# Performance work log

Measured on AMD Instinct MI355X. Metric: run time of the kernel, lower is better.

## Reference

```python
import jax, jax.numpy as jnp
import numpy as np

LORA_SCALING = 2.0


def setup_inputs() -> dict:
    key = jax.random.key(0)
    ks = jax.random.split(key, 12)
    B, S, H, F, E, R = 1, 2048, 2048, 8192, 8, 16
    s = 0.02  # small init so lora deltas stay numerically sane
    return {
        "hidden_states": jax.random.normal(ks[0], (B, S, H), jnp.float32),
        "gate_w": jax.random.normal(ks[1], (E, H), jnp.float32) * s,
        "Wg": jax.random.normal(ks[2], (F, H), jnp.float32) * s,
        "Wu": jax.random.normal(ks[3], (F, H), jnp.float32) * s,
        "Wd": jax.random.normal(ks[4], (H, F), jnp.float32) * s,
        "Ag": jax.random.normal(ks[5], (E, R, H), jnp.float32) * s,
        "Bg": jax.random.normal(ks[6], (E, F, R), jnp.float32) * s,
        "Au": jax.random.normal(ks[7], (E, R, H), jnp.float32) * s,
        "Bu": jax.random.normal(ks[8], (E, F, R), jnp.float32) * s,
        "Ad": jax.random.normal(ks[9], (E, R, F), jnp.float32) * s,
        "Bd": jax.random.normal(ks[10], (E, H, R), jnp.float32) * s,
        "top_k": 2,
    }


def reference(hidden_states, gate_w, Wg, Wu, Wd, Ag, Bg, Au, Bu, Ad, Bd, top_k):
    B, S, H = hidden_states.shape
    E = gate_w.shape[0]
    h = hidden_states.reshape(-1, H)  # [T, H]
    # router: softmax -> top-k -> renormalize
    logits = h @ gate_w.T                       # [T, E]
    rw = jax.nn.softmax(logits, axis=-1)
    rw_top, sel = jax.lax.top_k(rw, top_k)      # [T, K]
    rw_top = rw_top / jnp.sum(rw_top, axis=-1, keepdims=True)
    # per-token per-expert combine weight (0 if expert not selected)
    w_te = jnp.zeros((h.shape[0], E), h.dtype).at[
        jnp.arange(h.shape[0])[:, None], sel].add(rw_top)  # [T, E]
    # shared base projections computed once for all experts
    common_gate = h @ Wg.T   # [T, F]
    common_up = h @ Wu.T     # [T, F]
    out = jnp.zeros_like(h)
    for e in range(E):  # small fixed expert count; lora deltas are rank-16
        g = common_gate + LORA_SCALING * ((h @ Ag[e].T) @ Bg[e].T)
        u = common_up + LORA_SCALING * ((h @ Au[e].T) @ Bu[e].T)
        act = jax.nn.silu(g) * u                               # [T, F]
        d = act @ Wd.T + LORA_SCALING * ((act @ Ad[e].T) @ Bd[e].T)  # [T, H]
        out = out + w_te[:, e:e + 1] * d
    return out.reshape(B, S, H)
```

## Files before the change

### kernel.cpp

```cpp
#include <hip/hip_runtime.h>
#include <hip/hip_bf16.h>

typedef __attribute__((ext_vector_type(8))) short v8s;
typedef __attribute__((ext_vector_type(4))) float v4f;
typedef unsigned short u16;

static constexpr int TT = 2048;
static constexpr int HD = 2048;
static constexpr int FD = 8192;
static constexpr int NE = 8;
static constexpr int NR = 16;
static constexpr int NXE = 2*FD;
static constexpr int CU_OFF = FD;
static constexpr int KXD = FD + 512;

__device__ __forceinline__ u16 f2b(float f) {
  union { float f; unsigned u; } v; v.f = f;
  unsigned r = v.u + 0x7FFFu + ((v.u >> 16) & 1u);
  return (u16)(r >> 16);
}
__device__ __forceinline__ float b2f(u16 h) {
  union { unsigned u; float f; } v; v.u = ((unsigned)h) << 16;
  return v.f;
}
__device__ __forceinline__ v8s pack8(v4f a, v4f b) {
  v8s r;
  r[0]=(short)f2b(a.x); r[1]=(short)f2b(a.y); r[2]=(short)f2b(a.z); r[3]=(short)f2b(a.w);
  r[4]=(short)f2b(b.x); r[5]=(short)f2b(b.y); r[6]=(short)f2b(b.z); r[7]=(short)f2b(b.w);
  return r;
}
__device__ __forceinline__ void gload_lds16(const void* g, void* l) {
  __builtin_amdgcn_global_load_lds(
      (const __attribute__((address_space(1))) unsigned int*)g,
      (__attribute__((address_space(3))) unsigned int*)l, 16, 0, 0);
}
__device__ __forceinline__ void barrier_pin() {
  __builtin_amdgcn_s_barrier();
  __builtin_amdgcn_sched_barrier(0);
}
__device__ __forceinline__ void vm_wait4() { asm volatile("s_waitcnt vmcnt(4)" ::: "memory"); }
__device__ __forceinline__ void vm_wait0() { asm volatile("s_waitcnt vmcnt(0)" ::: "memory"); }

template<int Q>
__device__ __forceinline__ void mmq(v4f (&acc)[8][4], const v8s (&af)[2][2], const v8s (&bf)[4][2]) {
  __builtin_amdgcn_s_setprio(1);
  #pragma unroll
  for (int m2 = 0; m2 < 2; ++m2)
    #pragma unroll
    for (int nf = 0; nf < 4; ++nf) {
      acc[Q*2+m2][nf] = __builtin_amdgcn_mfma_f32_16x16x32_bf16(af[m2][0], bf[nf][0], acc[Q*2+m2][nf], 0, 0, 0);
      acc[Q*2+m2][nf] = __builtin_amdgcn_mfma_f32_16x16x32_bf16(af[m2][1], bf[nf][1], acc[Q*2+m2][nf], 0, 0, 0);
    }
  __builtin_amdgcn_s_setprio(0);
}

static constexpr int PREP_BLOCKS = 14592;
__global__ __launch_bounds__(256)
void prep_kernel(const float* __restrict__ h, const float* __restrict__ Wg,
                 const float* __restrict__ Wu, const float* __restrict__ Wd,
                 const float* __restrict__ Ag, const float* __restrict__ Au,
                 const float* __restrict__ Bg, const float* __restrict__ Bu,
                 const float* __restrict__ Ad, const float* __restrict__ Bd,
                 u16* __restrict__ hb, u16* __restrict__ Bgux, u16* __restrict__ Agu,
                 u16* __restrict__ Wdx, u16* __restrict__ Bgb, u16* __restrict__ Bub,
                 u16* __restrict__ Adb, float* __restrict__ hAx) {
  const int b = blockIdx.x, tid = threadIdx.x;
  auto cast16 = [&](const float* s, u16* d, long blk) {
    long i = blk*4096 + (long)tid*16;
    v4f a0 = *(const v4f*)(s+i),    a1 = *(const v4f*)(s+i+4);
    v4f a2 = *(const v4f*)(s+i+8),  a3 = *(const v4f*)(s+i+12);
    *(v8s*)(d+i)   = pack8(a0, a1);
    *(v8s*)(d+i+8) = pack8(a2, a3);
  };
  if (b < 1024) { cast16(h, hb, b); }
  else if (b < 5120)  { cast16(Wg, Bgux, b-1024); }
  else if (b < 9216)  { cast16(Wu, Bgux + (size_t)FD*HD, b-5120); }
  else if (b < 13312) {
    long idx = (long)(b-9216)*4096 + (long)tid*16;
    long r = idx >> 13; int c = (int)(idx & 8191);
    const float* s = Wd + r*FD + c;
    u16* d = Wdx + r*KXD + c;
    v4f a0 = *(const v4f*)s,     a1 = *(const v4f*)(s+4);
    v4f a2 = *(const v4f*)(s+8), a3 = *(const v4f*)(s+12);
    *(v8s*)d     = pack8(a0, a1);
    *(v8s*)(d+8) = pack8(a2, a3);
  }
  else if (b < 13376) { cast16(Ag, Agu, b-13312); }
  else if (b < 13440) { cast16(Au, Agu + (size_t)128*HD, b-13376); }
  else if (b < 13696) { cast16(Bg, Bgb, b-13440); }
  else if (b < 13952) { cast16(Bu, Bub, b-13696); }
  else if (b < 14208) { cast16(Ad, Adb, b-13952); }
  else if (b < 14464) {
    long idx = (long)(b-14208)*4096 + (long)tid*16;
    int hrow = (int)(idx >> 9); int c = (int)(idx & 511);
    u16* d = Wdx + (size_t)hrow*KXD + FD + c;
    if (c < 128) {
      const float* s = Bd + ((size_t)(c>>4)*HD + hrow)*16;
      v4f a0 = *(const v4f*)s,     a1 = *(const v4f*)(s+4);
      v4f a2 = *(const v4f*)(s+8), a3 = *(const v4f*)(s+12);
      *(v8s*)d     = pack8(a0, a1);
      *(v8s*)(d+8) = pack8(a2, a3);
    } else {
      v8s z = {0,0,0,0,0,0,0,0};
      *(v8s*)d = z; *(v8s*)(d+8) = z;
    }
  } else {
    long i = (long)(b-14464)*4096 + (long)tid*16;
    v4f z = {0.f,0.f,0.f,0.f};
    *(v4f*)(hAx+i) = z; *(v4f*)(hAx+i+4) = z;
    *(v4f*)(hAx+i+8) = z; *(v4f*)(hAx+i+12) = z;
  }
}

__global__ __launch_bounds__(64)
void router_kernel(const float* __restrict__ h, const float* __restrict__ gw,
                   int* __restrict__ sel, int* __restrict__ count,
                   int* __restrict__ listTok, float* __restrict__ listW) {
  int t = blockIdx.x, lane = threadIdx.x;
  const float* hp = h + (size_t)t * HD;
  float acc[8] = {0,0,0,0,0,0,0,0};
  for (int i = lane; i < HD; i += 64) {
    float hv = hp[i];
    #pragma unroll
    for (int e = 0; e < 8; ++e) acc[e] += hv * gw[e*HD + i];
  }
  #pragma unroll
  for (int off = 32; off > 0; off >>= 1) {
    #pragma unroll
    for (int e = 0; e < 8; ++e) acc[e] += __shfl_xor(acc[e], off, 64);
  }
  if (lane == 0) {
    int e0 = -1, e1 = -1; float b0 = -1e30f, b1 = -1e30f;
    #pragma unroll
    for (int e = 0; e < 8; ++e) {
      float v = acc[e];
      if (v > b0) { b1 = b0; e1 = e0; b0 = v; e0 = e; }
      else if (v > b1) { b1 = v; e1 = e; }
    }
    float p1 = __expf(b1 - b0);
    float w0 = 1.f / (1.f + p1);
    float w1 = p1 * w0;
    sel[2*t] = e0; sel[2*t+1] = e1;
    int pos0 = atomicAdd(&count[e0], 1);
    listTok[e0*TT + pos0] = t;           listW[e0*TT + pos0] = w0;
    int pos1 = atomicAdd(&count[e1], 1);
    listTok[e1*TT + pos1] = t | (1<<20); listW[e1*TT + pos1] = w1;
  }
}

__global__ __launch_bounds__(256)
void gemm128a(const u16* __restrict__ A, const u16* __restrict__ B, float* __restrict__ Cout,
              int K, int ldc) {
  __shared__ u16 As[128*64];
  __shared__ u16 Bs[128*64];
  const int tid  = threadIdx.x;
  const int lane = tid & 63, wid = tid >> 6;
  const int gx = gridDim.x;
  const int lin = blockIdx.y * gx + blockIdx.x;
  const int chunk = (gx * gridDim.y) >> 3;
  const int wg = (lin & 7) * chunk + (lin >> 3);
  const int m0 = (wg % gx) * 128, n0 = (wg / gx) * 128;
  const int kc = K / gridDim.z;
  const int kbeg = blockIdx.z * kc;
  const int wr = wid >> 1, wc = wid & 1;
  const int lrow = lane >> 3, lcol = (lane & 7) * 8;
  v4f acc[4][4];
  #pragma unroll
  for (int mi = 0; mi < 4; ++mi)
    #pragma unroll
    for (int ni = 0; ni < 4; ++ni) acc[mi][ni] = (v4f){0.f,0.f,0.f,0.f};

  for (int k0 = kbeg; k0 < kbeg + kc; k0 += 64) {
    #pragma unroll
    for (int it = 0; it < 4; ++it) {
      int seg = wid*4 + it;
      int row = seg*8 + lrow;
      gload_lds16(A + (size_t)(m0+row)*K + k0 + lcol, As + seg*512);
      gload_lds16(B + (size_t)(n0+row)*K + k0 + lcol, Bs + seg*512);
    }
    __syncthreads();
    #pragma unroll
    for (int kk = 0; kk < 64; kk += 32) {
      v8s af[4], bfr[4];
      #pragma unroll
      for (int mi = 0; mi < 4; ++mi)
        af[mi] = *(const v8s*)(As + (wr*64 + mi*16 + (lane&15))*64 + kk + (lane>>4)*8);
      #pragma unroll
      for (int ni = 0; ni < 4; ++ni)
        bfr[ni] = *(const v8s*)(Bs + (wc*64 + ni*16 + (lane&15))*64 + kk + (lane>>4)*8);
      #pragma unroll
      for (int mi = 0; mi < 4; ++mi)
        #pragma unroll
        for (int ni = 0; ni < 4; ++ni)
          acc[mi][ni] = __builtin_amdgcn_mfma_f32_16x16x32_bf16(af[mi], bfr[ni], acc[mi][ni], 0, 0, 0);
    }
    __syncthreads();
  }

  #pragma unroll
  for (int mi = 0; mi < 4; ++mi)
    #pragma unroll
    for (int j = 0; j < 4; ++j) {
      int row = m0 + wr*64 + mi*16 + (lane>>4)*4 + j;
      size_t base = (size_t)row*ldc + n0 + wc*64 + (lane&15);
      #pragma unroll
      for (int ni = 0; ni < 4; ++ni)
        atomicAdd(&Cout[base + ni*16], acc[mi][ni][j]);
    }
}

template<int MODE>
__global__ __launch_bounds__(512, 2)
void gemm256(const u16* __restrict__ A, const u16* __restrict__ B, void* __restrict__ Cout,
             int ldk, int kchunk, int ldc) {
  __shared__ u16 lds[2][2][2][8192];
  const int tid = threadIdx.x, lane = tid & 63, wid = tid >> 6;
  const int gx = gridDim.x;
  const int nwg = gx * gridDim.y;
  const int lin = blockIdx.y * gx + blockIdx.x;
  const int chunk = nwg >> 3;
  const int wg = (lin & 7) * chunk + (lin >> 3);
  const int m0 = (wg % gx) * 256, n0 = (wg / gx) * 256;
  const long kbeg = (long)blockIdx.z * kchunk;
  const int NK = kchunk >> 6, NI = NK >> 1;
  const int wr = wid >> 2, wc = wid & 3;

  const int s_r = (wid << 4) + (lane >> 3);
  const int s_c = lane & 7;

  auto STAGE = [&](int slot, int ab, int half, const u16* M, int rc0, int kt) {
    const u16* g0 = M + (size_t)(rc0 + half*128 + s_r) * ldk + kbeg + kt*64 + ((s_c ^ (s_r & 7)) << 3);
    gload_lds16(g0, &lds[slot][ab][half][wid << 10]);
    const int r1 = s_r + 8;
    const u16* g1 = M + (size_t)(rc0 + half*128 + r1) * ldk + kbeg + kt*64 + ((s_c ^ (r1 & 7)) << 3);
    gload_lds16(g1, &lds[slot][ab][half][(wid << 10) + 512]);
  };
  auto LDA = [&](int slot, int mf, int c16b) -> v8s {
    int rr = (mf << 4) + (lane & 15);
    return *(const v8s*)&lds[slot][0][wr][rr*64 + (((c16b + (lane >> 4)) ^ (rr & 7)) << 3)];
  };
  auto LDB = [&](int slot, int nf, int c16b) -> v8s {
    int row = (wc << 6) + (nf << 4) + (lane & 15);
    int rr = row & 127;
    return *(const v8s*)&lds[slot][1][row >> 7][rr*64 + (((c16b + (lane >> 4)) ^ (rr & 7)) << 3)];
  };

  v4f acc[8][4];
  #pragma unroll
  for (int mf = 0; mf < 8; ++mf)
    #pragma unroll
    for (int nf = 0; nf < 4; ++nf) acc[mf][nf] = (v4f){0.f,0.f,0.f,0.f};

  STAGE(0,1,0,B,n0,0); STAGE(0,1,1,B,n0,0);
  STAGE(0,0,0,A,m0,0); STAGE(0,0,1,A,m0,0);
  STAGE(1,1,0,B,n0,1); STAGE(1,1,1,B,n0,1);
  vm_wait4();
  barrier_pin();

  for (int i = 0; i < NI; ++i) {
    const int kt0 = 2*i, kt1 = kt0 + 1;
    const int kt2c = (kt0 + 2 < NK) ? kt0 + 2 : kt0;
    const bool s45 = (kt0 + 2 < NK), s67 = (kt1 + 2 < NK);
    v8s bf[4][2], af[2][2];
    #pragma unroll
    for (int nf = 0; nf < 4; ++nf) { bf[nf][0] = LDB(0,nf,0); bf[nf][1] = LDB(0,nf,4); }
    af[0][0]=LDA(0,0,0); af[0][1]=LDA(0,0,4); af[1][0]=LDA(0,1,0); af[1][1]=LDA(0,1,4);
    STAGE(1,0,0,A,m0,kt1);
    barrier_pin(); mmq<0>(acc,af,bf); barrier_pin();
    af[0][0]=LDA(0,2,0); af[0][1]=LDA(0,2,4); af[1][0]=LDA(0,3,0); af[1][1]=LDA(0,3,4);
    STAGE(1,0,1,A,m0,kt1);
    barrier_pin(); mmq<1>(acc,af,bf); barrier_pin();
    af[0][0]=LDA(0,4,0); af[0][1]=LDA(0,4,4); af[1][0]=LDA(0,5,0); af[1][1]=LDA(0,5,4);
    STAGE(0,1,0,B,n0,kt2c);
    barrier_pin(); mmq<2>(acc,af,bf); barrier_pin();
    af[0][0]=LDA(0,6,0); af[0][1]=LDA(0,6,4); af[1][0]=LDA(0,7,0); af[1][1]=LDA(0,7,4);
    STAGE(0,1,1,B,n0,kt2c);
    vm_wait4();
    barrier_pin(); mmq<3>(acc,af,bf); barrier_pin();
    #pragma unroll
    for (int nf = 0; nf < 4; ++nf) { bf[nf][0] = LDB(1,nf,0); bf[nf][1] = LDB(1,nf,4); }
    af[0][0]=LDA(1,0,0); af[0][1]=LDA(1,0,4); af[1][0]=LDA(1,1,0); af[1][1]=LDA(1,1,4);
    if (s45) STAGE(0,0,0,A,m0,kt0+2);
    barrier_pin(); mmq<0>(acc,af,bf); barrier_pin();
    af[0][0]=LDA(1,2,0); af[0][1]=LDA(1,2,4); af[1][0]=LDA(1,3,0); af[1][1]=LDA(1,3,4);
    if (s45) STAGE(0,0,1,A,m0,kt0+2);
    barrier_pin(); mmq<1>(acc,af,bf); barrier_pin();
    af[0][0]=LDA(1,4,0); af[0][1]=LDA(1,4,4); af[1][0]=LDA(1,5,0); af[1][1]=LDA(1,5,4);
    if (s67) STAGE(1,1,0,B,n0,kt1+2);
    barrier_pin(); mmq<2>(acc,af,bf); barrier_pin();
    af[0][0]=LDA(1,6,0); af[0][1]=LDA(1,6,4); af[1][0]=LDA(1,7,0); af[1][1]=LDA(1,7,4);
    if (s67) STAGE(1,1,1,B,n0,kt1+2);
    vm_wait4();
    barrier_pin(); mmq<3>(acc,af,bf); barrier_pin();
  }
  vm_wait0();

  if (MODE == 0) {
    u16* C = (u16*)Cout;
    #pragma unroll
    for (int mf = 0; mf < 8; ++mf)
      #pragma unroll
      for (int j = 0; j < 4; ++j) {
        int row = m0 + wr*128 + mf*16 + (lane>>4)*4 + j;
        size_t base = (size_t)row*ldc + n0 + wc*64 + (lane&15);
        #pragma unroll
        for (int nf = 0; nf < 4; ++nf)
          C[base + nf*16] = f2b(acc[mf][nf][j]);
      }
  } else {
    float* C = (float*)Cout + (size_t)blockIdx.z * TT * HD;
    #pragma unroll
    for (int mf = 0; mf < 8; ++mf)
      #pragma unroll
      for (int j = 0; j < 4; ++j) {
        int row = m0 + wr*128 + mf*16 + (lane>>4)*4 + j;
        size_t base = (size_t)row*ldc + n0 + wc*64 + (lane&15);
        #pragma unroll
        for (int nf = 0; nf < 4; ++nf)
          C[base + nf*16] = acc[mf][nf][j];
      }
  }
}

__global__ __launch_bounds__(256)
void reduce4_kernel(const float* __restrict__ P, float* __restrict__ out) {
  long i = ((long)blockIdx.x * 256 + threadIdx.x) * 4;
  const size_t S = (size_t)TT * HD;
  v4f s = *(const v4f*)(P + i);
  s = s + *(const v4f*)(P + S + i);
  s = s + *(const v4f*)(P + 2*S + i);
  s = s + *(const v4f*)(P + 3*S + i);
  *(v4f*)(out + i) = s;
}

static constexpr int HA_LD = 40;
static constexpr int AW_LD = 72;
static constexpr int CT_LD = 72;

__global__ __launch_bounds__(256)
void expert_kernel(const u16* __restrict__ CGU,
                   const float* __restrict__ hAx,
                   const u16* __restrict__ Bgb, const u16* __restrict__ Bub,
                   const u16* __restrict__ Adb,
                   const int* __restrict__ count, const int* __restrict__ listTok,
                   const float* __restrict__ listW,
                   u16* __restrict__ actw0, u16* __restrict__ actw1,
                   float* __restrict__ cC) {
  const int e = blockIdx.y, g = blockIdx.x, fb = blockIdx.z;
  const int n = count[e];
  if (g*16 >= n) return;
  const int tid = threadIdx.x, lane = tid & 63, w = tid >> 6;
  __shared__ u16 hAg[16*HA_LD], hAu[16*HA_LD];
  __shared__ u16 AWs[4][16*AW_LD];
  __shared__ u16 cgT[4][16*CT_LD], cuT[4][16*CT_LD];
  __shared__ int sTok[16], sSlot[16];
  __shared__ float sW[16];
  __shared__ float dAred[4][256];

  if (tid < 16) {
    int idx = g*16 + tid;
    if (idx < n) {
      int ent = listTok[e*TT + idx];
      sTok[tid] = ent & 0xFFFF; sSlot[tid] = (ent >> 20) & 1; sW[tid] = listW[e*TT + idx];
    } else { sTok[tid] = TT; sSlot[tid] = 0; sW[tid] = 0.f; }
  }
  __syncthreads();
  if (tid < 128) {
    int tensor = tid >> 6;
    int sub = tid & 63;
    int row = sub >> 2, c8 = (sub & 3) * 8;
    int trd = min(sTok[row], TT - 1);
    u16 vals[8];
    if (c8 < 16) {
      const float* src = hAx + (size_t)trd*256 + tensor*128 + e*NR + c8;
      v4f a = *(const v4f*)src, b = *(const v4f*)(src + 4);
      v8s p = pack8(a, b);
      #pragma unroll
      for (int q = 0; q < 8; ++q) vals[q] = (u16)p[q];
    } else {
      #pragma unroll
      for (int q = 0; q < 8; ++q) vals[q] = 0;
    }
    u16* dst = (tensor ? hAu : hAg) + row*HA_LD + c8;
    #pragma unroll
    for (int q = 0; q < 8; ++q) dst[q] = vals[q];
  }
  __syncthreads();

  int tR[4], slR[4]; float wR[4];
  #pragma unroll
  for (int j = 0; j < 4; ++j) {
    int r = (lane>>4)*4 + j;
    tR[j] = sTok[r]; slR[j] = sSlot[r]; wR[j] = sW[r];
  }
  const int khalf = lane >> 4;
  v8s afg = *(const v8s*)(hAg + (lane&15)*HA_LD + khalf*8);
  v8s afu = *(const v8s*)(hAu + (lane&15)*HA_LD + khalf*8);
  v4f accDA = (v4f){0.f,0.f,0.f,0.f};
  u16* aww = AWs[w]; u16* cgw = cgT[w]; u16* cuw = cuT[w];
  const v8s zero8 = {0,0,0,0,0,0,0,0};
  const u16* BgE = Bgb + (size_t)e*FD*16;
  const u16* BuE = Bub + (size_t)e*FD*16;
  const u16* AdE = Adb + (size_t)e*16*FD;

  const int srj = lane >> 2, sc = (lane & 3) * 16;

  const int srow = lane >> 3, c8s = (lane & 7) * 8;
  const size_t trdA = (size_t)min(sTok[srow], TT - 1);
  const size_t trdB = (size_t)min(sTok[srow + 8], TT - 1);
  v8s rg0, rg1, ru0, ru1;
  auto LOADC = [&](int f0) {
    rg0 = *(const v8s*)(CGU + trdA*NXE + f0 + c8s);
    ru0 = *(const v8s*)(CGU + trdA*NXE + CU_OFF + f0 + c8s);
    rg1 = *(const v8s*)(CGU + trdB*NXE + f0 + c8s);
    ru1 = *(const v8s*)(CGU + trdB*NXE + CU_OFF + f0 + c8s);
  };
  auto WRITEC = [&]() {
    *(v8s*)(cgw + srow*CT_LD + c8s)     = rg0;
    *(v8s*)(cgw + (srow+8)*CT_LD + c8s) = rg1;
    *(v8s*)(cuw + srow*CT_LD + c8s)     = ru0;
    *(v8s*)(cuw + (srow+8)*CT_LD + c8s) = ru1;
  };

  const int ch_beg = fb*32 + w, ch_end = fb*32 + 32;
  LOADC(ch_beg * 64);
  WRITEC();
  for (int ch = ch_beg; ch < ch_end; ch += 4) {
    int f0 = ch * 64;
    const bool pf = (ch + 4 < ch_end);
    if (pf) LOADC((ch + 4) * 64);
    v4f dg[4], du[4];
    #pragma unroll
    for (int nf = 0; nf < 4; ++nf) {
      int f = f0 + nf*16 + (lane & 15);
      v8s bgf = (khalf < 2) ? *(const v8s*)(BgE + (size_t)f*16 + khalf*8) : zero8;
      dg[nf] = __builtin_amdgcn_mfma_f32_16x16x32_bf16(afg, bgf, (v4f){0.f,0.f,0.f,0.f}, 0, 0, 0);
      v8s buf = (khalf < 2) ? *(const v8s*)(BuE + (size_t)f*16 + khalf*8) : zero8;
      du[nf] = __builtin_amdgcn_mfma_f32_16x16x32_bf16(afu, buf, (v4f){0.f,0.f,0.f,0.f}, 0, 0, 0);
    }
    #pragma unroll
    for (int nf = 0; nf < 4; ++nf) {
      #pragma unroll
      for (int j = 0; j < 4; ++j) {
        int rj = (lane>>4)*4 + j;
        int fi = nf*16 + (lane&15);
        float cgv = b2f(cgw[rj*CT_LD + fi]);
        float cuv = b2f(cuw[rj*CT_LD + fi]);
        float gv = cgv + 2.f * dg[nf][j];
        float uv = cuv + 2.f * du[nf][j];
        float a  = gv * __builtin_amdgcn_rcpf(1.f + __expf(-gv)) * uv;
        aww[rj*AW_LD + fi] = f2b(wR[j] * a);
      }
    }
    {
      int st = sTok[srj], ss = sSlot[srj];
      u16* dst = (ss ? actw1 : actw0) + (size_t)st*FD + f0 + sc;
      *(v8s*)dst       = *(const v8s*)(aww + srj*AW_LD + sc);
      *(v8s*)(dst + 8) = *(const v8s*)(aww + srj*AW_LD + sc + 8);
    }
    #pragma unroll
    for (int ks = 0; ks < 2; ++ks) {
      v8s aA = *(const v8s*)(aww + (lane&15)*AW_LD + ks*32 + khalf*8);
      v8s bA = *(const v8s*)(AdE + (size_t)(lane&15)*FD + f0 + ks*32 + khalf*8);
      accDA = __builtin_amdgcn_mfma_f32_16x16x32_bf16(aA, bA, accDA, 0, 0, 0);
    }
    if (pf) WRITEC();
  }
  #pragma unroll
  for (int j = 0; j < 4; ++j)
    dAred[w][((lane>>4)*4 + j)*16 + (lane&15)] = accDA[j];
  __syncthreads();
  {
    int row = tid >> 4, col = tid & 15;
    float s2 = dAred[0][row*16+col] + dAred[1][row*16+col] + dAred[2][row*16+col] + dAred[3][row*16+col];
    atomicAdd(&cC[((size_t)sTok[row]*2 + sSlot[row])*16 + col], 2.f * s2);
  }
}

__global__ __launch_bounds__(256)
void combine2_kernel(const u16* __restrict__ a0, const u16* __restrict__ a1,
                     const float* __restrict__ cC, const int* __restrict__ sel,
                     u16* __restrict__ abx) {
  int t = blockIdx.x, tid = threadIdx.x;
  const u16* p0 = a0 + (size_t)t * FD;
  const u16* p1 = a1 + (size_t)t * FD;
  u16* po = abx + (size_t)t * KXD;
  for (int i = tid * 8; i < FD; i += 256 * 8) {
    v8s x = *(const v8s*)(p0 + i);
    v8s y = *(const v8s*)(p1 + i);
    v8s o;
    #pragma unroll
    for (int j = 0; j < 8; ++j) o[j] = (short)f2b(b2f((u16)x[j]) + b2f((u16)y[j]));
    *(v8s*)(po + i) = o;
  }
  for (int c = tid; c < 512; c += 256) {
    float v = 0.f;
    if (c < 128) {
      int e_i = c >> 4, r = c & 15;
      if (sel[2*t]     == e_i) v += cC[((size_t)t*2 + 0)*16 + r];
      if (sel[2*t + 1] == e_i) v += cC[((size_t)t*2 + 1)*16 + r];
    }
    po[FD + c] = f2b(v);
  }
}

extern "C" void kernel_launch(void* const* d_in, const int* in_sizes, int n_in,
                              void* d_out, int out_size, void* d_ws, size_t ws_size,
                              hipStream_t stream) {
  (void)in_sizes; (void)n_in; (void)out_size; (void)ws_size;
  const float* h  = (const float*)d_in[0];
  const float* gw = (const float*)d_in[1];
  const float* Wg = (const float*)d_in[2];
  const float* Wu = (const float*)d_in[3];
  const float* Wd = (const float*)d_in[4];
  const float* Ag = (const float*)d_in[5];
  const float* Bg = (const float*)d_in[6];
  const float* Au = (const float*)d_in[7];
  const float* Bu = (const float*)d_in[8];
  const float* Ad = (const float*)d_in[9];
  const float* Bd = (const float*)d_in[10];

  char* ws = (char*)d_ws;
  size_t off = 0;
  auto alloc = [&](size_t bytes) { size_t c = off; off += (bytes + 255) & ~(size_t)255; return c; };
  u16*  hb     = (u16*)(ws + alloc((size_t)TT*HD*2));
  u16*  Bgux   = (u16*)(ws + alloc((size_t)(TT+1)*FD*2*2));
  u16*  Agu    = (u16*)(ws + alloc((size_t)256*HD*2));
  u16*  Wdx    = (u16*)(ws + alloc((size_t)HD*KXD*2));
  u16*  CGU    = (u16*)(ws + alloc((size_t)TT*NXE*2));
  u16*  Bgb    = (u16*)(ws + alloc((size_t)NE*FD*16*2));
  u16*  Bub    = (u16*)(ws + alloc((size_t)NE*FD*16*2));
  u16*  Adb    = (u16*)(ws + alloc((size_t)NE*16*FD*2));
  float* hAx   = (float*)(ws + alloc((size_t)TT*256*4));
  float* cC    = (float*)(ws + alloc((size_t)(TT+1)*2*16*4));
  int*  sel    = (int*)(ws + alloc((size_t)TT*2*4));
  int*  count  = (int*)(ws + alloc(256));
  int*  listTok= (int*)(ws + alloc((size_t)NE*TT*4));
  float* listW = (float*)(ws + alloc((size_t)NE*TT*4));
  u16*  actw0  = Bgux;
  u16*  actw1  = Bgux + (size_t)(TT+1)*FD;
  u16*  abx    = CGU;
  float* parts = (float*)Bgux;

  hipMemsetAsync(count, 0, NE*sizeof(int), stream);
  hipMemsetAsync(cC, 0, (size_t)(TT+1)*2*16*4, stream);

  prep_kernel<<<PREP_BLOCKS, 256, 0, stream>>>(h, Wg, Wu, Wd, Ag, Au, Bg, Bu, Ad, Bd,
                                               hb, Bgux, Agu, Wdx, Bgb, Bub, Adb, hAx);

  router_kernel<<<TT, 64, 0, stream>>>(h, gw, sel, count, listTok, listW);

  gemm128a<<<dim3(16, 2, 8), 256, 0, stream>>>(hb, Agu, hAx, HD, 256);

  gemm256<0><<<dim3(8, 32, 1), 512, 0, stream>>>(hb, Bgux, CGU, HD, HD, NXE);
  gemm256<0><<<dim3(8, 32, 1), 512, 0, stream>>>(hb, Bgux + (size_t)FD*HD, CGU + CU_OFF, HD, HD, NXE);

  expert_kernel<<<dim3(128, NE, 4), 256, 0, stream>>>(CGU, hAx, Bgb, Bub, Adb, count, listTok, listW,
                                                      actw0, actw1, cC);

  combine2_kernel<<<TT, 256, 0, stream>>>(actw0, actw1, cC, sel, abx);

  gemm256<3><<<dim3(8, 8, 4), 512, 0, stream>>>(abx, Wdx, parts, KXD, KXD/4, HD);

  reduce4_kernel<<<4096, 256, 0, stream>>>(parts, (float*)d_out);
}
```

Baseline: 456.0 us.

## Double-buffer expert kernel loads, split F across more blocks, widen prep casts

The expert kernel now preloads all global operands for a chunk (Bg/Bu fragments, Ad fragments, and the common gate/up values) into a register struct. It double-buffers these across a fully unrolled sequence of four chunks, so loads for the next chunk are in flight while the current one computes. The F dimension is split over twice as many blocks (grid z 4 to 8, 16 chunks per block instead of 32), which raises parallelism but repeats the per-block setup and atomics more often. The prep cast kernel handles 32 elements per thread instead of 16, halving its block count. The extra register state may reduce occupancy.

```diff
diff --git a/kernel.cpp b/kernel.cpp
--- a/kernel.cpp
+++ b/kernel.cpp
@@ -54,7 +54,7 @@
   __builtin_amdgcn_s_setprio(0);
 }
 
-static constexpr int PREP_BLOCKS = 14592;
+static constexpr int PREP_BLOCKS = 7424;
 __global__ __launch_bounds__(256)
 void prep_kernel(const float* __restrict__ h, const float* __restrict__ Wg,
                  const float* __restrict__ Wu, const float* __restrict__ Wd,
@@ -65,33 +65,35 @@
                  u16* __restrict__ Wdx, u16* __restrict__ Bgb, u16* __restrict__ Bub,
                  u16* __restrict__ Adb, float* __restrict__ hAx) {
   const int b = blockIdx.x, tid = threadIdx.x;
-  auto cast16 = [&](const float* s, u16* d, long blk) {
-    long i = blk*4096 + (long)tid*16;
-    v4f a0 = *(const v4f*)(s+i),    a1 = *(const v4f*)(s+i+4);
-    v4f a2 = *(const v4f*)(s+i+8),  a3 = *(const v4f*)(s+i+12);
-    *(v8s*)(d+i)   = pack8(a0, a1);
-    *(v8s*)(d+i+8) = pack8(a2, a3);
-  };
-  if (b < 1024) { cast16(h, hb, b); }
-  else if (b < 5120)  { cast16(Wg, Bgux, b-1024); }
-  else if (b < 9216)  { cast16(Wu, Bgux + (size_t)FD*HD, b-5120); }
-  else if (b < 13312) {
-    long idx = (long)(b-9216)*4096 + (long)tid*16;
+  auto cast32at = [&](const float* s, u16* d) {
+    v4f a0 = *(const v4f*)(s),    a1 = *(const v4f*)(s+4);
+    v4f a2 = *(const v4f*)(s+8),  a3 = *(const v4f*)(s+12);
+    v4f a4 = *(const v4f*)(s+16), a5 = *(const v4f*)(s+20);
+    v4f a6 = *(const v4f*)(s+24), a7 = *(const v4f*)(s+28);
+    *(v8s*)(d)    = pack8(a0, a1);
+    *(v8s*)(d+8)  = pack8(a2, a3);
+    *(v8s*)(d+16) = pack8(a4, a5);
+    *(v8s*)(d+24) = pack8(a6, a7);
+  };
+  auto cast32 = [&](const float* s, u16* d, long blk) {
+    long i = blk*8192 + (long)tid*32;
+    cast32at(s+i, d+i);
+  };
+  if (b < 512) { cast32(h, hb, b); }
+  else if (b < 2560) { cast32(Wg, Bgux, b-512); }
+  else if (b < 4608) { cast32(Wu, Bgux + (size_t)FD*HD, b-2560); }
+  else if (b < 6656) {
+    long idx = (long)(b-4608)*8192 + (long)tid*32;
     long r = idx >> 13; int c = (int)(idx & 8191);
-    const float* s = Wd + r*FD + c;
-    u16* d = Wdx + r*KXD + c;
-    v4f a0 = *(const v4f*)s,     a1 = *(const v4f*)(s+4);
-    v4f a2 = *(const v4f*)(s+8), a3 = *(const v4f*)(s+12);
-    *(v8s*)d     = pack8(a0, a1);
-    *(v8s*)(d+8) = pack8(a2, a3);
-  }
-  else if (b < 13376) { cast16(Ag, Agu, b-13312); }
-  else if (b < 13440) { cast16(Au, Agu + (size_t)128*HD, b-13376); }
-  else if (b < 13696) { cast16(Bg, Bgb, b-13440); }
-  else if (b < 13952) { cast16(Bu, Bub, b-13696); }
-  else if (b < 14208) { cast16(Ad, Adb, b-13952); }
-  else if (b < 14464) {
-    long idx = (long)(b-14208)*4096 + (long)tid*16;
+    cast32at(Wd + r*FD + c, Wdx + r*KXD + c);
+  }
+  else if (b < 6688) { cast32(Ag, Agu, b-6656); }
+  else if (b < 6720) { cast32(Au, Agu + (size_t)128*HD, b-6688); }
+  else if (b < 6848) { cast32(Bg, Bgb, b-6720); }
+  else if (b < 6976) { cast32(Bu, Bub, b-6848); }
+  else if (b < 7104) { cast32(Ad, Adb, b-6976); }
+  else if (b < 7360) {
+    long idx = (long)(b-7104)*4096 + (long)tid*16;
     int hrow = (int)(idx >> 9); int c = (int)(idx & 511);
     u16* d = Wdx + (size_t)hrow*KXD + FD + c;
     if (c < 128) {
@@ -105,10 +107,10 @@
       *(v8s*)d = z; *(v8s*)(d+8) = z;
     }
   } else {
-    long i = (long)(b-14464)*4096 + (long)tid*16;
+    long i = (long)(b-7360)*8192 + (long)tid*32;
     v4f z = {0.f,0.f,0.f,0.f};
-    *(v4f*)(hAx+i) = z; *(v4f*)(hAx+i+4) = z;
-    *(v4f*)(hAx+i+8) = z; *(v4f*)(hAx+i+12) = z;
+    #pragma unroll
+    for (int q = 0; q < 8; ++q) *(v4f*)(hAx+i+q*4) = z;
   }
 }
 
@@ -336,6 +338,11 @@
 static constexpr int HA_LD = 40;
 static constexpr int AW_LD = 72;
 static constexpr int CT_LD = 72;
+
+struct PF {
+  v8s bg[4], bu[4], ad[2];
+  v8s rg0, ru0, rg1, ru1;
+};
 
 __global__ __launch_bounds__(256)
 void expert_kernel(const u16* __restrict__ CGU,
@@ -404,39 +411,38 @@
   const u16* AdE = Adb + (size_t)e*16*FD;
 
   const int srj = lane >> 2, sc = (lane & 3) * 16;
-
   const int srow = lane >> 3, c8s = (lane & 7) * 8;
   const size_t trdA = (size_t)min(sTok[srow], TT - 1);
   const size_t trdB = (size_t)min(sTok[srow + 8], TT - 1);
-  v8s rg0, rg1, ru0, ru1;
-  auto LOADC = [&](int f0) {
-    rg0 = *(const v8s*)(CGU + trdA*NXE + f0 + c8s);
-    ru0 = *(const v8s*)(CGU + trdA*NXE + CU_OFF + f0 + c8s);
-    rg1 = *(const v8s*)(CGU + trdB*NXE + f0 + c8s);
-    ru1 = *(const v8s*)(CGU + trdB*NXE + CU_OFF + f0 + c8s);
-  };
-  auto WRITEC = [&]() {
-    *(v8s*)(cgw + srow*CT_LD + c8s)     = rg0;
-    *(v8s*)(cgw + (srow+8)*CT_LD + c8s) = rg1;
-    *(v8s*)(cuw + srow*CT_LD + c8s)     = ru0;
-    *(v8s*)(cuw + (srow+8)*CT_LD + c8s) = ru1;
-  };
-
-  const int ch_beg = fb*32 + w, ch_end = fb*32 + 32;
-  LOADC(ch_beg * 64);
-  WRITEC();
-  for (int ch = ch_beg; ch < ch_end; ch += 4) {
-    int f0 = ch * 64;
-    const bool pf = (ch + 4 < ch_end);
-    if (pf) LOADC((ch + 4) * 64);
-    v4f dg[4], du[4];
+
+  auto LOADPF = [&](int ch, PF& p) {
+    const int f0 = ch * 64;
     #pragma unroll
     for (int nf = 0; nf < 4; ++nf) {
       int f = f0 + nf*16 + (lane & 15);
-      v8s bgf = (khalf < 2) ? *(const v8s*)(BgE + (size_t)f*16 + khalf*8) : zero8;
-      dg[nf] = __builtin_amdgcn_mfma_f32_16x16x32_bf16(afg, bgf, (v4f){0.f,0.f,0.f,0.f}, 0, 0, 0);
-      v8s buf = (khalf < 2) ? *(const v8s*)(BuE + (size_t)f*16 + khalf*8) : zero8;
-      du[nf] = __builtin_amdgcn_mfma_f32_16x16x32_bf16(afu, buf, (v4f){0.f,0.f,0.f,0.f}, 0, 0, 0);
+      p.bg[nf] = (khalf < 2) ? *(const v8s*)(BgE + (size_t)f*16 + khalf*8) : zero8;
+      p.bu[nf] = (khalf < 2) ? *(const v8s*)(BuE + (size_t)f*16 + khalf*8) : zero8;
+    }
+    #pragma unroll
+    for (int ks = 0; ks < 2; ++ks)
+      p.ad[ks] = *(const v8s*)(AdE + (size_t)(lane&15)*FD + f0 + ks*32 + khalf*8);
+    p.rg0 = *(const v8s*)(CGU + trdA*NXE + f0 + c8s);
+    p.ru0 = *(const v8s*)(CGU + trdA*NXE + CU_OFF + f0 + c8s);
+    p.rg1 = *(const v8s*)(CGU + trdB*NXE + f0 + c8s);
+    p.ru1 = *(const v8s*)(CGU + trdB*NXE + CU_OFF + f0 + c8s);
+  };
+
+  auto COMPUTE = [&](int ch, const PF& p) {
+    const int f0 = ch * 64;
+    *(v8s*)(cgw + srow*CT_LD + c8s)     = p.rg0;
+    *(v8s*)(cgw + (srow+8)*CT_LD + c8s) = p.rg1;
+    *(v8s*)(cuw + srow*CT_LD + c8s)     = p.ru0;
+    *(v8s*)(cuw + (srow+8)*CT_LD + c8s) = p.ru1;
+    v4f dg[4], du[4];
+    #pragma unroll
+    for (int nf = 0; nf < 4; ++nf) {
+      dg[nf] = __builtin_amdgcn_mfma_f32_16x16x32_bf16(afg, p.bg[nf], (v4f){0.f,0.f,0.f,0.f}, 0, 0, 0);
+      du[nf] = __builtin_amdgcn_mfma_f32_16x16x32_bf16(afu, p.bu[nf], (v4f){0.f,0.f,0.f,0.f}, 0, 0, 0);
     }
     #pragma unroll
     for (int nf = 0; nf < 4; ++nf) {
@@ -461,11 +467,21 @@
     #pragma unroll
     for (int ks = 0; ks < 2; ++ks) {
       v8s aA = *(const v8s*)(aww + (lane&15)*AW_LD + ks*32 + khalf*8);
-      v8s bA = *(const v8s*)(AdE + (size_t)(lane&15)*FD + f0 + ks*32 + khalf*8);
-      accDA = __builtin_amdgcn_mfma_f32_16x16x32_bf16(aA, bA, accDA, 0, 0, 0);
-    }
-    if (pf) WRITEC();
-  }
+      accDA = __builtin_amdgcn_mfma_f32_16x16x32_bf16(aA, p.ad[ks], accDA, 0, 0, 0);
+    }
+  };
+
+  const int ch0 = fb*16 + w;
+  PF pA, pB;
+  LOADPF(ch0,      pA);
+  LOADPF(ch0 + 4,  pB);
+  COMPUTE(ch0,     pA);
+  LOADPF(ch0 + 8,  pA);
+  COMPUTE(ch0 + 4, pB);
+  LOADPF(ch0 + 12, pB);
+  COMPUTE(ch0 + 8, pA);
+  COMPUTE(ch0 + 12, pB);
+
   #pragma unroll
   for (int j = 0; j < 4; ++j)
     dAred[w][((lane>>4)*4 + j)*16 + (lane&15)] = accDA[j];
@@ -555,7 +571,7 @@
   gemm256<0><<<dim3(8, 32, 1), 512, 0, stream>>>(hb, Bgux, CGU, HD, HD, NXE);
   gemm256<0><<<dim3(8, 32, 1), 512, 0, stream>>>(hb, Bgux + (size_t)FD*HD, CGU + CU_OFF, HD, HD, NXE);
 
-  expert_kernel<<<dim3(128, NE, 4), 256, 0, stream>>>(CGU, hAx, Bgb, Bub, Adb, count, listTok, listW,
+  expert_kernel<<<dim3(128, NE, 8), 256, 0, stream>>>(CGU, hAx, Bgb, Bub, Adb, count, listTok, listW,
                                                       actw0, actw1, cC);
 
   combine2_kernel<<<TT, 256, 0, stream>>>(actw0, actw1, cC, sel, abx);
```

After: 453.7 us. Within noise of the previous version (-0.5%).
